# Performance work log

Measured on AMD Instinct MI355X. Metric: run time of the kernel, lower is better.

Reference implementation:

```python
import math
import jax, jax.numpy as jnp
import numpy as np

B, T, C, H = 4, 2048, 1024, 16
D = C // H  # head dim = 64


def setup_inputs() -> dict:
    key = jax.random.key(0)
    ks = jax.random.split(key, 5)
    s = 1.0 / math.sqrt(C)
    return {
        "x": jax.random.normal(ks[0], (B, T, C), jnp.float32),
        "w_qkv": jax.random.normal(ks[1], (C, 3 * C), jnp.float32) * s,
        "b_qkv": jax.random.normal(ks[2], (3 * C,), jnp.float32) * 0.02,
        "w_out": jax.random.normal(ks[3], (C, C), jnp.float32) * s,
        "b_out": jax.random.normal(ks[4], (C,), jnp.float32) * 0.02,
    }


def reference(x, w_qkv, b_qkv, w_out, b_out):
    # qkv projection: (B,T,C) @ (C,3C) -> split into Q,K,V
    qkv = x @ w_qkv + b_qkv
    q, k, v = jnp.split(qkv, 3, axis=-1)
    # reshape to (B,H,T,D)
    q = q.reshape(B, T, H, D).transpose(0, 2, 1, 3)
    k = k.reshape(B, T, H, D).transpose(0, 2, 1, 3)
    v = v.reshape(B, T, H, D).transpose(0, 2, 1, 3)
    # scaled scores with causal mask
    scores = jnp.einsum("bhqd,bhkd->bhqk", q, k) * (1.0 / math.sqrt(D))
    causal = jnp.tril(jnp.ones((T, T), dtype=bool))
    scores = jnp.where(causal[None, None], scores, -jnp.inf)
    attn = jax.nn.softmax(scores, axis=-1)  # dropout_rate=0 (eval)
    out = jnp.einsum("bhqk,bhkd->bhqd", attn, v)
    out = out.transpose(0, 2, 1, 3).reshape(B, T, C)
    return out @ w_out + b_out
```

## Files before the change

### kernel.cpp

```cpp
#include <hip/hip_runtime.h>
#include <cstdint>
#include <cstddef>

typedef _Float16 h8_t __attribute__((ext_vector_type(8)));
typedef _Float16 h4_t __attribute__((ext_vector_type(4)));
typedef float f32x4 __attribute__((ext_vector_type(4)));
typedef float f32x16 __attribute__((ext_vector_type(16)));
typedef unsigned u32x4 __attribute__((ext_vector_type(4)));

#define MFMA_16x16x32_F16(a, b, c) __builtin_amdgcn_mfma_f32_16x16x32_f16(a, b, c, 0, 0, 0)
#define MFMA_32x32x16_F16(a, b, c) __builtin_amdgcn_mfma_f32_32x32x16_f16(a, b, c, 0, 0, 0)

__device__ inline void gload_lds16(const void* g, void* l) {
  __builtin_amdgcn_global_load_lds((const __attribute__((address_space(1))) void*)g,
                                   (__attribute__((address_space(3))) void*)l, 16, 0, 0);
}

#define CFENCE asm volatile("" ::: "memory")
#define RAW_BAR() do { CFENCE; __builtin_amdgcn_s_barrier(); CFENCE; } while (0)

__global__ void cvt_f16_kernel(const float* __restrict__ in, _Float16* __restrict__ out, int n4) {
  int i = blockIdx.x * 256 + threadIdx.x;
  if (i >= n4) return;
  float4 v = reinterpret_cast<const float4*>(in)[i];
  h4_t h;
  h[0] = (_Float16)v.x; h[1] = (_Float16)v.y; h[2] = (_Float16)v.z; h[3] = (_Float16)v.w;
  reinterpret_cast<h4_t*>(out)[i] = h;
}

__global__ void transpose_cvt_kernel(const float* __restrict__ in, _Float16* __restrict__ out,
                                     int R, int Cc) {
  __shared__ float tile[32][33];
  int tx = threadIdx.x & 31;
  int ty = threadIdx.x >> 5;
  int c0 = blockIdx.x * 32;
  int r0 = blockIdx.y * 32;
#pragma unroll
  for (int i = 0; i < 4; ++i)
    tile[ty + i * 8][tx] = in[(size_t)(r0 + ty + i * 8) * Cc + (c0 + tx)];
  __syncthreads();
#pragma unroll
  for (int i = 0; i < 4; ++i)
    out[(size_t)(c0 + ty + i * 8) * R + (r0 + tx)] = (_Float16)tile[tx][ty + i * 8];
}

__global__ __launch_bounds__(512, 2) void gemm_qkv_kernel(
    const _Float16* __restrict__ A, const _Float16* __restrict__ Bt,
    const float* __restrict__ bias, _Float16* __restrict__ outQ,
    _Float16* __restrict__ outK, _Float16* __restrict__ outV) {
  __shared__ _Float16 Al[3][8192];
  __shared__ _Float16 Bl[3][12288];

  const int tid = threadIdx.x;
  const int lane = tid & 63;
  const int w = tid >> 6;
  const int wm = w >> 2, wn = w & 3;
  const int bm = blockIdx.x >> 3;
  const int bn = blockIdx.x & 7;
  const int m0 = bm * 256;
  const int n0 = bn * 384;

  f32x4 acc[8][6];
#pragma unroll
  for (int i = 0; i < 8; ++i)
#pragma unroll
    for (int j = 0; j < 6; ++j) acc[i][j] = (f32x4){0.f, 0.f, 0.f, 0.f};

  const int fg0 = tid >> 6;
  const int sl = tid & 63;
  const int srow = fg0 * 16 + (sl & 15);
  const int scol = (sl >> 4) * 8;
  const _Float16* aS = A + (size_t)(m0 + srow) * 1024 + scol;
  const _Float16* bS = Bt + (size_t)(n0 + srow) * 1024 + scol;
  const int sdst = tid * 8;

  auto stageA = [&](int buf, int kt) {
    const int k0 = kt * 32;
    gload_lds16(aS + k0, &Al[buf][sdst]);
    gload_lds16(aS + 131072 + k0, &Al[buf][sdst + 4096]);
  };
  auto stageB = [&](int buf, int kt) {
    const int k0 = kt * 32;
    gload_lds16(bS + k0, &Bl[buf][sdst]);
    gload_lds16(bS + 131072 + k0, &Bl[buf][sdst + 4096]);
    gload_lds16(bS + 262144 + k0, &Bl[buf][sdst + 8192]);
  };

  const int offA0 = (wm * 8 * 64 + lane) * 8;
  const int offB0 = (wn * 6 * 64 + lane) * 8;

  stageA(0, 0); stageB(0, 0);
  stageA(1, 1); stageB(1, 1);
  asm volatile("s_waitcnt vmcnt(5)" ::: "memory");
  RAW_BAR();

  int cur = 0;
#pragma unroll 1
  for (int t = 0; t < 32; ++t) {
    int nb = cur + 2; if (nb >= 3) nb -= 3;
    const bool st = (t + 2) < 32;
    const _Float16* Ab = &Al[cur][0];
    const _Float16* Bb = &Bl[cur][0];
    h8_t af[4], bf[6];

#pragma unroll
    for (int mf = 0; mf < 4; ++mf) af[mf] = *(const h8_t*)&Ab[offA0 + mf * 512];
#pragma unroll
    for (int nf = 0; nf < 6; ++nf) bf[nf] = *(const h8_t*)&Bb[offB0 + nf * 512];
    if (st) stageA(nb, t + 2);
    RAW_BAR();
    asm volatile("s_waitcnt lgkmcnt(0)" ::: "memory");
    __builtin_amdgcn_sched_barrier(0);
    __builtin_amdgcn_s_setprio(1);
#pragma unroll
    for (int mf = 0; mf < 4; ++mf)
#pragma unroll
      for (int nf = 0; nf < 6; ++nf)
        acc[mf][nf] = MFMA_16x16x32_F16(af[mf], bf[nf], acc[mf][nf]);
    __builtin_amdgcn_s_setprio(0);
    RAW_BAR();

#pragma unroll
    for (int mf = 0; mf < 4; ++mf) af[mf] = *(const h8_t*)&Ab[offA0 + (4 + mf) * 512];
    if (st) stageB(nb, t + 2);
    RAW_BAR();
    asm volatile("s_waitcnt lgkmcnt(0)" ::: "memory");
    __builtin_amdgcn_sched_barrier(0);
    __builtin_amdgcn_s_setprio(1);
#pragma unroll
    for (int mf = 0; mf < 4; ++mf)
#pragma unroll
      for (int nf = 0; nf < 6; ++nf)
        acc[4 + mf][nf] = MFMA_16x16x32_F16(af[mf], bf[nf], acc[4 + mf][nf]);
    __builtin_amdgcn_s_setprio(0);
    if (t < 31) {
      if (st) asm volatile("s_waitcnt vmcnt(5)" ::: "memory");
      else asm volatile("s_waitcnt vmcnt(0)" ::: "memory");
      RAW_BAR();
    }
    ++cur; if (cur == 3) cur = 0;
  }

  const int gm0 = m0 + wm * 128;
  const int gn0 = n0 + wn * 96;
#pragma unroll
  for (int mf = 0; mf < 8; ++mf) {
#pragma unroll
    for (int nf = 0; nf < 6; ++nf) {
      const int gn = gn0 + nf * 16 + (lane & 15);
      const int tm0 = gm0 + mf * 16 + (lane >> 4) * 4;
      const float bv = bias[gn];
      const int which = gn >> 10;
      const int nn = gn & 1023;
      const int h = nn >> 6, d = nn & 63;
      const int t0 = tm0 & 2047, b = tm0 >> 11;
      const int bh = b * 16 + h;
      if (which == 2) {
        h4_t pack;
#pragma unroll
        for (int r = 0; r < 4; ++r) pack[r] = (_Float16)(acc[mf][nf][r] + bv);
        *reinterpret_cast<h4_t*>(&outV[((size_t)bh * 64 + d) * 2048 + t0]) = pack;
      } else {
        _Float16* dst = (which == 0) ? outQ : outK;
        const float scale = (which == 0) ? 0.18033688011112042f : 1.0f;
#pragma unroll
        for (int r = 0; r < 4; ++r)
          dst[((size_t)bh * 2048 + t0 + r) * 64 + d] = (_Float16)((acc[mf][nf][r] + bv) * scale);
      }
    }
  }
}

__global__ __launch_bounds__(256, 3) void gemm_out_kernel(
    const _Float16* __restrict__ A, const _Float16* __restrict__ Bt,
    const float* __restrict__ bias, float* __restrict__ outF, int NB) {
  __shared__ _Float16 Al[3][4096];
  __shared__ _Float16 Bl[3][4096];
  const int tid = threadIdx.x;
  const int lane = tid & 63;
  const int w = tid >> 6;
  const int bm = blockIdx.x / NB;
  const int bn = blockIdx.x % NB;
  const int wm = w & 1, wn = w >> 1;
  const int m0 = bm * 128, n0 = bn * 128;

  f32x4 acc[4][4];
#pragma unroll
  for (int m = 0; m < 4; ++m)
#pragma unroll
    for (int n = 0; n < 4; ++n) acc[m][n] = (f32x4){0.f, 0.f, 0.f, 0.f};

  const int seg0 = w * 2, seg1 = w * 2 + 1;
  const int r0s = seg0 * 16 + (lane >> 2);
  const int r1s = seg1 * 16 + (lane >> 2);
  const int c0s = ((lane & 3) ^ ((r0s >> 1) & 3)) * 8;
  const int c1s = ((lane & 3) ^ ((r1s >> 1) & 3)) * 8;
  const _Float16* aS0 = A + (size_t)(m0 + r0s) * 1024 + c0s;
  const _Float16* aS1 = A + (size_t)(m0 + r1s) * 1024 + c1s;
  const _Float16* bS0 = Bt + (size_t)(n0 + r0s) * 1024 + c0s;
  const _Float16* bS1 = Bt + (size_t)(n0 + r1s) * 1024 + c1s;
  const int d0 = seg0 * 512 + lane * 8;
  const int d1 = seg1 * 512 + lane * 8;

  auto stage = [&](int buf, int kt) {
    const int k0 = kt * 32;
    gload_lds16(aS0 + k0, &Al[buf][d0]);
    gload_lds16(bS0 + k0, &Bl[buf][d0]);
    gload_lds16(aS1 + k0, &Al[buf][d1]);
    gload_lds16(bS1 + k0, &Bl[buf][d1]);
  };

  int offA[4], offB[4];
#pragma unroll
  for (int i = 0; i < 4; ++i) {
    const int rowA = wm * 64 + i * 16 + (lane & 15);
    offA[i] = rowA * 32 + (((lane >> 4) ^ ((rowA >> 1) & 3)) * 8);
    const int rowB = wn * 64 + i * 16 + (lane & 15);
    offB[i] = rowB * 32 + (((lane >> 4) ^ ((rowB >> 1) & 3)) * 8);
  }

  stage(0, 0);
  stage(1, 1);
  asm volatile("s_waitcnt vmcnt(4)" ::: "memory");
  RAW_BAR();

  int cur = 0;
#pragma unroll 1
  for (int t = 0; t < 32; ++t) {
    int nb = cur + 2; if (nb >= 3) nb -= 3;
    if (t + 2 < 32) stage(nb, t + 2);
    const _Float16* Ab = &Al[cur][0];
    const _Float16* Bb = &Bl[cur][0];
    h8_t af[4], bf[4];
#pragma unroll
    for (int i = 0; i < 4; ++i) af[i] = *(const h8_t*)&Ab[offA[i]];
#pragma unroll
    for (int j = 0; j < 4; ++j) bf[j] = *(const h8_t*)&Bb[offB[j]];
#pragma unroll
    for (int i = 0; i < 4; ++i)
#pragma unroll
      for (int j = 0; j < 4; ++j)
        acc[i][j] = MFMA_16x16x32_F16(af[i], bf[j], acc[i][j]);
    if (t < 31) {
      if (t + 2 < 32) asm volatile("s_waitcnt vmcnt(4)" ::: "memory");
      else asm volatile("s_waitcnt vmcnt(0)" ::: "memory");
      RAW_BAR();
    }
    ++cur; if (cur == 3) cur = 0;
  }

  const int gm0 = bm * 128 + wm * 64;
  const int gn0 = bn * 128 + wn * 64;
#pragma unroll
  for (int i = 0; i < 4; ++i) {
#pragma unroll
    for (int j = 0; j < 4; ++j) {
      const int gn = gn0 + j * 16 + (lane & 15);
      const int tm0 = gm0 + i * 16 + (lane >> 4) * 4;
      const float bv = bias[gn];
#pragma unroll
      for (int r = 0; r < 4; ++r)
        outF[(size_t)(tm0 + r) * 1024 + gn] = acc[i][j][r] + bv;
    }
  }
}

__device__ inline void stage_kv64(const _Float16* __restrict__ Kbh, const _Float16* __restrict__ Vbh,
                                  int kt, _Float16* Kd, _Float16* Vd, int w, int lane) {
  const _Float16* Kg = Kbh + (size_t)kt * 64 * 64;
  const _Float16* Vg = Vbh + kt * 64;
#pragma unroll
  for (int c = 0; c < 2; ++c) {
    const int idx = (2 * w + c) * 64 + lane;
    const int row = idx >> 3;
    const int chs = (idx & 7) ^ (row & 7);
    gload_lds16(Kg + row * 64 + chs * 8, Kd + idx * 8);
    gload_lds16(Vg + (size_t)row * 2048 + chs * 8, Vd + idx * 8);
  }
}

__device__ inline void pack_pfrag(const float* e, h8_t* out) {
  unsigned u[8];
#pragma unroll
  for (int i = 0; i < 8; ++i) {
    auto hv = __builtin_amdgcn_cvt_pkrtz(e[2 * i], e[2 * i + 1]);
    u[i] = __builtin_bit_cast(unsigned, hv);
  }
  auto r02 = __builtin_amdgcn_permlane32_swap(u[0], u[2], false, false);
  auto r13 = __builtin_amdgcn_permlane32_swap(u[1], u[3], false, false);
  auto r46 = __builtin_amdgcn_permlane32_swap(u[4], u[6], false, false);
  auto r57 = __builtin_amdgcn_permlane32_swap(u[5], u[7], false, false);
  u32x4 w0 = {(unsigned)r02[0], (unsigned)r13[0], (unsigned)r02[1], (unsigned)r13[1]};
  u32x4 w1 = {(unsigned)r46[0], (unsigned)r57[0], (unsigned)r46[1], (unsigned)r57[1]};
  out[0] = __builtin_bit_cast(h8_t, w0);
  out[1] = __builtin_bit_cast(h8_t, w1);
}

__global__ __launch_bounds__(256, 2) void attn_kernel(
    const _Float16* __restrict__ Q, const _Float16* __restrict__ K,
    const _Float16* __restrict__ Vt, _Float16* __restrict__ O) {
  __shared__ _Float16 Kl[2][2][64 * 64];
  __shared__ _Float16 Vl[2][2][64 * 64];
  const int tid = threadIdx.x;
  const int lane = tid & 63;
  const int w = tid >> 6;
  const int hi = lane >> 5;
  const int l31 = lane & 31;
  const int bh = blockIdx.x & 63;
  const int pr = blockIdx.x >> 6;
  const int b = bh >> 4, h = bh & 15;
  const _Float16* Kbh = K + (size_t)bh * 2048 * 64;
  const _Float16* Vbh = Vt + (size_t)bh * 64 * 2048;

#pragma unroll
  for (int gi = 0; gi < 2; ++gi) {
    const int g = gi ? (15 - pr) : pr;
    const int nT = g + 1;
    const int qbase = g * 128 + w * 32;
    const int qrow = qbase + l31;

    h8_t qf[4];
    const _Float16* Qp = Q + ((size_t)bh * 2048 + qrow) * 64 + hi * 8;
#pragma unroll
    for (int ds = 0; ds < 4; ++ds)
      qf[ds] = *reinterpret_cast<const h8_t*>(Qp + ds * 16);

    f32x16 oa[2] = {};
    float m = -1e30f, lsum = 0.f;

    stage_kv64(Kbh, Vbh, 0, &Kl[0][0][0], &Vl[0][0][0], w, lane);
    stage_kv64(Kbh, Vbh, 1, &Kl[0][1][0], &Vl[0][1][0], w, lane);
    __syncthreads();

#pragma unroll 1
    for (int T = 0; T < nT; ++T) {
      const int cur = T & 1;
      if (T + 1 < nT) {
        stage_kv64(Kbh, Vbh, 2 * (T + 1), &Kl[cur ^ 1][0][0], &Vl[cur ^ 1][0][0], w, lane);
        stage_kv64(Kbh, Vbh, 2 * (T + 1) + 1, &Kl[cur ^ 1][1][0], &Vl[cur ^ 1][1][0], w, lane);
      }

      const bool diag = (T == g);
      const bool skip1 = diag && (w < 2);
      f32x16 s[2][2];

#pragma unroll
      for (int half = 0; half < 2; ++half) {
        if (half == 1 && skip1) {
#pragma unroll
          for (int r = 0; r < 16; ++r) { s[1][0][r] = -1e30f; s[1][1][r] = -1e30f; }
        } else {
          const char* Kb = (const char*)&Kl[cur][half][0];
          f32x16 a0 = {}, a1 = {};
#pragma unroll
          for (int ds = 0; ds < 4; ++ds) {
            const int bc = ds * 32 + hi * 16;
            h8_t kf0 = *(const h8_t*)(Kb + l31 * 128 + (bc ^ ((l31 & 7) << 4)));
            h8_t kf1 = *(const h8_t*)(Kb + (32 + l31) * 128 + (bc ^ ((l31 & 7) << 4)));
            a0 = MFMA_32x32x16_F16(kf0, qf[ds], a0);
            a1 = MFMA_32x32x16_F16(kf1, qf[ds], a1);
          }
          s[half][0] = a0;
          s[half][1] = a1;
        }
      }
      if (diag) {
#pragma unroll
        for (int half = 0; half < 2; ++half) {
          if (half == 1 && skip1) continue;
#pragma unroll
          for (int r = 0; r < 16; ++r) {
            const int kr = T * 128 + half * 64 + (r & 3) + 8 * (r >> 2) + 4 * hi;
            if (kr > qrow) s[half][0][r] = -1e30f;
            if (kr + 32 > qrow) s[half][1][r] = -1e30f;
          }
        }
      }

      float t[16];
#pragma unroll
      for (int r = 0; r < 16; ++r)
        t[r] = fmaxf(fmaxf(s[0][0][r], s[0][1][r]), fmaxf(s[1][0][r], s[1][1][r]));
#pragma unroll
      for (int st = 8; st >= 1; st >>= 1)
#pragma unroll
        for (int r = 0; r < st; ++r) t[r] = fmaxf(t[r], t[r + st]);
      const float pmax = fmaxf(t[0], __shfl_xor(t[0], 32));
      const float mnew = fmaxf(m, pmax);
      if (__any(mnew > m + 8.f)) {
        const float al = __builtin_amdgcn_exp2f(m - mnew);
        lsum *= al;
#pragma unroll
        for (int r = 0; r < 16; ++r) { oa[0][r] *= al; oa[1][r] *= al; }
        m = mnew;
      }
      float ps = 0.f;
#pragma unroll
      for (int half = 0; half < 2; ++half)
#pragma unroll
        for (int sub = 0; sub < 2; ++sub)
#pragma unroll
          for (int r = 0; r < 16; ++r) {
            const float pv = __builtin_amdgcn_exp2f(s[half][sub][r] - m);
            s[half][sub][r] = pv;
            ps += pv;
          }
      ps += __shfl_xor(ps, 32);
      lsum += ps;

#pragma unroll
      for (int half = 0; half < 2; ++half) {
        if (half == 1 && skip1) continue;
        h8_t pf[4];
        pack_pfrag((const float*)&s[half][0], pf + 0);
        pack_pfrag((const float*)&s[half][1], pf + 2);
        const char* Vb = (const char*)&Vl[cur][half][0];
#pragma unroll
        for (int dt = 0; dt < 2; ++dt) {
#pragma unroll
          for (int kg = 0; kg < 4; ++kg) {
            const int row = dt * 32 + l31;
            const int bc = kg * 32 + hi * 16;
            h8_t vf = *(const h8_t*)(Vb + row * 128 + (bc ^ ((row & 7) << 4)));
            oa[dt] = MFMA_32x32x16_F16(vf, pf[kg], oa[dt]);
          }
        }
      }
      __syncthreads();
    }

    const float inv = __builtin_amdgcn_rcpf(lsum);
    _Float16* Op = O + ((size_t)b * 2048 + qrow) * 1024 + h * 64;
#pragma unroll
    for (int dt = 0; dt < 2; ++dt) {
#pragma unroll
      for (int rg = 0; rg < 4; ++rg) {
        h4_t pk4;
#pragma unroll
        for (int i = 0; i < 4; ++i) pk4[i] = (_Float16)(oa[dt][rg * 4 + i] * inv);
        *reinterpret_cast<h4_t*>(Op + dt * 32 + rg * 8 + hi * 4) = pk4;
      }
    }
  }
}

extern "C" void kernel_launch(void* const* d_in, const int* in_sizes, int n_in,
                              void* d_out, int out_size, void* d_ws, size_t ws_size,
                              hipStream_t stream) {
  (void)in_sizes; (void)n_in; (void)out_size; (void)ws_size;
  const float* x = (const float*)d_in[0];
  const float* w_qkv = (const float*)d_in[1];
  const float* b_qkv = (const float*)d_in[2];
  const float* w_out = (const float*)d_in[3];
  const float* b_out = (const float*)d_in[4];
  float* out = (float*)d_out;

  char* ws = (char*)d_ws;
  size_t off = 0;
  auto alloc = [&](size_t bytes) {
    void* p = ws + off;
    off += (bytes + 255) & ~(size_t)255;
    return p;
  };
  _Float16* x16 = (_Float16*)alloc((size_t)8192 * 1024 * 2);
  _Float16* wqkvT = (_Float16*)alloc((size_t)3072 * 1024 * 2);
  _Float16* woutT = (_Float16*)alloc((size_t)1024 * 1024 * 2);
  _Float16* Qh = (_Float16*)alloc((size_t)64 * 2048 * 64 * 2);
  _Float16* Kh = (_Float16*)alloc((size_t)64 * 2048 * 64 * 2);
  _Float16* Vth = (_Float16*)alloc((size_t)64 * 64 * 2048 * 2);
  _Float16* Oh = (_Float16*)alloc((size_t)8192 * 1024 * 2);

  cvt_f16_kernel<<<8192, 256, 0, stream>>>(x, x16, 8192 * 1024 / 4);
  transpose_cvt_kernel<<<dim3(3072 / 32, 1024 / 32), 256, 0, stream>>>(w_qkv, wqkvT, 1024, 3072);
  transpose_cvt_kernel<<<dim3(1024 / 32, 1024 / 32), 256, 0, stream>>>(w_out, woutT, 1024, 1024);
  gemm_qkv_kernel<<<256, 512, 0, stream>>>(x16, wqkvT, b_qkv, Qh, Kh, Vth);
  attn_kernel<<<64 * 8, 256, 0, stream>>>(Qh, Kh, Vth, Oh);
  gemm_out_kernel<<<64 * 8, 256, 0, stream>>>(Oh, woutT, b_out, out, 8);
}
```

Before: 171.5 us.

## Fuse x fp16 conversion into QKV GEMM loads and merge weight prep kernels

Drops the separate x-to-fp16 conversion kernel. The QKV GEMM now loads fp32 x into registers, converts to fp16 and writes it to LDS itself, and its main loop is restructured so prefetch is issued at the top with fewer barriers. The two weight transpose kernels are merged into one launch, and s_setprio is raised around the MFMA blocks in attention. This removes a full 32MB read plus a 16MB write and two launches, in exchange for register-staged A loads and more VALU work inside the GEMM.

Result: slower. 206.4 us (+20.4%).

```diff
diff --git a/kernel.cpp b/kernel.cpp
--- a/kernel.cpp
+++ b/kernel.cpp
@@ -19,33 +19,30 @@
 #define CFENCE asm volatile("" ::: "memory")
 #define RAW_BAR() do { CFENCE; __builtin_amdgcn_s_barrier(); CFENCE; } while (0)
 
-__global__ void cvt_f16_kernel(const float* __restrict__ in, _Float16* __restrict__ out, int n4) {
-  int i = blockIdx.x * 256 + threadIdx.x;
-  if (i >= n4) return;
-  float4 v = reinterpret_cast<const float4*>(in)[i];
-  h4_t h;
-  h[0] = (_Float16)v.x; h[1] = (_Float16)v.y; h[2] = (_Float16)v.z; h[3] = (_Float16)v.w;
-  reinterpret_cast<h4_t*>(out)[i] = h;
-}
-
-__global__ void transpose_cvt_kernel(const float* __restrict__ in, _Float16* __restrict__ out,
-                                     int R, int Cc) {
+__global__ void prep_kernel(const float* __restrict__ wqkv, _Float16* __restrict__ wqkvT,
+                            const float* __restrict__ wout, _Float16* __restrict__ woutT) {
   __shared__ float tile[32][33];
+  int blk = blockIdx.x;
+  const float* src;
+  _Float16* dst;
+  int Cc, cb, rb;
+  if (blk < 3072) { src = wqkv; dst = wqkvT; Cc = 3072; cb = blk % 96; rb = blk / 96; }
+  else { blk -= 3072; src = wout; dst = woutT; Cc = 1024; cb = blk & 31; rb = blk >> 5; }
+  const int R = 1024;
   int tx = threadIdx.x & 31;
   int ty = threadIdx.x >> 5;
-  int c0 = blockIdx.x * 32;
-  int r0 = blockIdx.y * 32;
+  int c0 = cb * 32, r0 = rb * 32;
 #pragma unroll
   for (int i = 0; i < 4; ++i)
-    tile[ty + i * 8][tx] = in[(size_t)(r0 + ty + i * 8) * Cc + (c0 + tx)];
+    tile[ty + i * 8][tx] = src[(size_t)(r0 + ty + i * 8) * Cc + (c0 + tx)];
   __syncthreads();
 #pragma unroll
   for (int i = 0; i < 4; ++i)
-    out[(size_t)(c0 + ty + i * 8) * R + (r0 + tx)] = (_Float16)tile[tx][ty + i * 8];
+    dst[(size_t)(c0 + ty + i * 8) * R + (r0 + tx)] = (_Float16)tile[tx][ty + i * 8];
 }
 
 __global__ __launch_bounds__(512, 2) void gemm_qkv_kernel(
-    const _Float16* __restrict__ A, const _Float16* __restrict__ Bt,
+    const float* __restrict__ X, const _Float16* __restrict__ Bt,
     const float* __restrict__ bias, _Float16* __restrict__ outQ,
     _Float16* __restrict__ outK, _Float16* __restrict__ outV) {
   __shared__ _Float16 Al[3][8192];
@@ -70,14 +67,34 @@
   const int sl = tid & 63;
   const int srow = fg0 * 16 + (sl & 15);
   const int scol = (sl >> 4) * 8;
-  const _Float16* aS = A + (size_t)(m0 + srow) * 1024 + scol;
+  const float* aS0 = X + (size_t)(m0 + srow) * 1024 + scol;
+  const float* aS1 = aS0 + 131072;
   const _Float16* bS = Bt + (size_t)(n0 + srow) * 1024 + scol;
   const int sdst = tid * 8;
 
-  auto stageA = [&](int buf, int kt) {
-    const int k0 = kt * 32;
-    gload_lds16(aS + k0, &Al[buf][sdst]);
-    gload_lds16(aS + 131072 + k0, &Al[buf][sdst + 4096]);
+  f32x4 ar0, ar1, ar2, ar3;
+
+  auto issueA = [&](int kt) {
+    const float* p0 = aS0 + kt * 32;
+    const float* p1 = aS1 + kt * 32;
+    asm volatile(
+        "global_load_dwordx4 %0, %4, off\n\t"
+        "global_load_dwordx4 %1, %4, off offset:16\n\t"
+        "global_load_dwordx4 %2, %5, off\n\t"
+        "global_load_dwordx4 %3, %5, off offset:16"
+        : "=&v"(ar0), "=&v"(ar1), "=&v"(ar2), "=&v"(ar3)
+        : "v"(p0), "v"(p1)
+        : "memory");
+  };
+  auto writeA = [&](int buf) {
+    h8_t h0, h1;
+#pragma unroll
+    for (int i = 0; i < 4; ++i) {
+      h0[i] = (_Float16)ar0[i]; h0[4 + i] = (_Float16)ar1[i];
+      h1[i] = (_Float16)ar2[i]; h1[4 + i] = (_Float16)ar3[i];
+    }
+    *reinterpret_cast<h8_t*>(&Al[buf][sdst]) = h0;
+    *reinterpret_cast<h8_t*>(&Al[buf][sdst + 4096]) = h1;
   };
   auto stageB = [&](int buf, int kt) {
     const int k0 = kt * 32;
@@ -89,9 +106,17 @@
   const int offA0 = (wm * 8 * 64 + lane) * 8;
   const int offB0 = (wn * 6 * 64 + lane) * 8;
 
-  stageA(0, 0); stageB(0, 0);
-  stageA(1, 1); stageB(1, 1);
-  asm volatile("s_waitcnt vmcnt(5)" ::: "memory");
+  issueA(0);
+  stageB(0, 0);
+  asm volatile("s_waitcnt vmcnt(3)" ::: "memory");
+  __builtin_amdgcn_sched_barrier(0);
+  writeA(0);
+  issueA(1);
+  stageB(1, 1);
+  asm volatile("s_waitcnt vmcnt(3)" ::: "memory");
+  __builtin_amdgcn_sched_barrier(0);
+  writeA(1);
+  asm volatile("s_waitcnt lgkmcnt(0)" ::: "memory");
   RAW_BAR();
 
   int cur = 0;
@@ -103,12 +128,12 @@
     const _Float16* Bb = &Bl[cur][0];
     h8_t af[4], bf[6];
 
+    if (st) { issueA(t + 2); stageB(nb, t + 2); }
+
 #pragma unroll
     for (int mf = 0; mf < 4; ++mf) af[mf] = *(const h8_t*)&Ab[offA0 + mf * 512];
 #pragma unroll
     for (int nf = 0; nf < 6; ++nf) bf[nf] = *(const h8_t*)&Bb[offB0 + nf * 512];
-    if (st) stageA(nb, t + 2);
-    RAW_BAR();
     asm volatile("s_waitcnt lgkmcnt(0)" ::: "memory");
     __builtin_amdgcn_sched_barrier(0);
     __builtin_amdgcn_s_setprio(1);
@@ -118,12 +143,9 @@
       for (int nf = 0; nf < 6; ++nf)
         acc[mf][nf] = MFMA_16x16x32_F16(af[mf], bf[nf], acc[mf][nf]);
     __builtin_amdgcn_s_setprio(0);
-    RAW_BAR();
 
 #pragma unroll
     for (int mf = 0; mf < 4; ++mf) af[mf] = *(const h8_t*)&Ab[offA0 + (4 + mf) * 512];
-    if (st) stageB(nb, t + 2);
-    RAW_BAR();
     asm volatile("s_waitcnt lgkmcnt(0)" ::: "memory");
     __builtin_amdgcn_sched_barrier(0);
     __builtin_amdgcn_s_setprio(1);
@@ -133,9 +155,16 @@
       for (int nf = 0; nf < 6; ++nf)
         acc[4 + mf][nf] = MFMA_16x16x32_F16(af[mf], bf[nf], acc[4 + mf][nf]);
     __builtin_amdgcn_s_setprio(0);
+
     if (t < 31) {
-      if (st) asm volatile("s_waitcnt vmcnt(5)" ::: "memory");
-      else asm volatile("s_waitcnt vmcnt(0)" ::: "memory");
+      if (st) {
+        asm volatile("s_waitcnt vmcnt(3)" ::: "memory");
+        __builtin_amdgcn_sched_barrier(0);
+        writeA(nb);
+      } else {
+        asm volatile("s_waitcnt vmcnt(0)" ::: "memory");
+      }
+      asm volatile("s_waitcnt lgkmcnt(0)" ::: "memory");
       RAW_BAR();
     }
     ++cur; if (cur == 3) cur = 0;
@@ -344,6 +373,7 @@
       const bool skip1 = diag && (w < 2);
       f32x16 s[2][2];
 
+      __builtin_amdgcn_s_setprio(1);
 #pragma unroll
       for (int half = 0; half < 2; ++half) {
         if (half == 1 && skip1) {
@@ -364,6 +394,7 @@
           s[half][1] = a1;
         }
       }
+      __builtin_amdgcn_s_setprio(0);
       if (diag) {
 #pragma unroll
         for (int half = 0; half < 2; ++half) {
@@ -415,6 +446,7 @@
         pack_pfrag((const float*)&s[half][0], pf + 0);
         pack_pfrag((const float*)&s[half][1], pf + 2);
         const char* Vb = (const char*)&Vl[cur][half][0];
+        __builtin_amdgcn_s_setprio(1);
 #pragma unroll
         for (int dt = 0; dt < 2; ++dt) {
 #pragma unroll
@@ -425,6 +457,7 @@
             oa[dt] = MFMA_32x32x16_F16(vf, pf[kg], oa[dt]);
           }
         }
+        __builtin_amdgcn_s_setprio(0);
       }
       __syncthreads();
     }
@@ -462,7 +495,6 @@
     off += (bytes + 255) & ~(size_t)255;
     return p;
   };
-  _Float16* x16 = (_Float16*)alloc((size_t)8192 * 1024 * 2);
   _Float16* wqkvT = (_Float16*)alloc((size_t)3072 * 1024 * 2);
   _Float16* woutT = (_Float16*)alloc((size_t)1024 * 1024 * 2);
   _Float16* Qh = (_Float16*)alloc((size_t)64 * 2048 * 64 * 2);
@@ -470,10 +502,8 @@
   _Float16* Vth = (_Float16*)alloc((size_t)64 * 64 * 2048 * 2);
   _Float16* Oh = (_Float16*)alloc((size_t)8192 * 1024 * 2);
 
-  cvt_f16_kernel<<<8192, 256, 0, stream>>>(x, x16, 8192 * 1024 / 4);
-  transpose_cvt_kernel<<<dim3(3072 / 32, 1024 / 32), 256, 0, stream>>>(w_qkv, wqkvT, 1024, 3072);
-  transpose_cvt_kernel<<<dim3(1024 / 32, 1024 / 32), 256, 0, stream>>>(w_out, woutT, 1024, 1024);
-  gemm_qkv_kernel<<<256, 512, 0, stream>>>(x16, wqkvT, b_qkv, Qh, Kh, Vth);
+  prep_kernel<<<4096, 256, 0, stream>>>(w_qkv, wqkvT, w_out, woutT);
+  gemm_qkv_kernel<<<256, 512, 0, stream>>>(x, wqkvT, b_qkv, Qh, Kh, Vth);
   attn_kernel<<<64 * 8, 256, 0, stream>>>(Qh, Kh, Vth, Oh);
   gemm_out_kernel<<<64 * 8, 256, 0, stream>>>(Oh, woutT, b_out, out, 8);
 }
```
